# Kernel optimization log

Hardware: AMD Instinct MI355X
Metric: run time of the kernel (lower is better)

Reference implementation:

```python
import jax, jax.numpy as jnp
import numpy as np
from jax import lax

DIM = 96
D_STATE = 16
D_CONV = 4
EXPAND = 2
D_INNER = EXPAND * DIM           # 192
DT_RANK = (DIM + 15) // 16       # 6
EPS = 1e-5


def _upsample2x_align_corners(x):
    # bilinear, align_corners=True, scale_factor=2 (matches nn.Upsample)
    B, C, H, W = x.shape
    def lin_idx(n_in, n_out):
        pos = jnp.arange(n_out) * ((n_in - 1) / (n_out - 1))
        i0 = jnp.floor(pos).astype(jnp.int32)
        i1 = jnp.minimum(i0 + 1, n_in - 1)
        w = (pos - i0).astype(x.dtype)
        return i0, i1, w
    r0, r1, rw = lin_idx(H, 2 * H)
    c0, c1, cw = lin_idx(W, 2 * W)
    xr = x[:, :, r0, :] * (1 - rw)[None, None, :, None] + x[:, :, r1, :] * rw[None, None, :, None]
    return xr[:, :, :, c0] * (1 - cw) + xr[:, :, :, c1] * cw


def _conv2d(x, w, b, pad):
    y = lax.conv_general_dilated(x, w, (1, 1), [(pad, pad), (pad, pad)],
                                 dimension_numbers=('NCHW', 'OIHW', 'NCHW'))
    return y + b[None, :, None, None]


def _instance_norm(x):
    m = x.mean(axis=(2, 3), keepdims=True)
    v = x.var(axis=(2, 3), keepdims=True)
    return (x - m) * lax.rsqrt(v + EPS)


def _selective_scan(u, dt, A, Bm, Cm, D):
    # u, dt: [B,L,Din]; Bm, Cm: [B,L,N]; A: [Din,N]; D: [Din]
    def step(h, inp):
        u_t, dt_t, B_t, C_t = inp                       # [B,Din],[B,Din],[B,N],[B,N]
        dA = jnp.exp(dt_t[..., None] * A)               # [B,Din,N]
        h = h * dA + (dt_t * u_t)[..., None] * B_t[:, None, :]
        y = jnp.einsum('bdn,bn->bd', h, C_t)
        return h, y
    Bsz, L, Din = u.shape
    h0 = jnp.zeros((Bsz, Din, A.shape[1]), u.dtype)
    xs = (u.swapaxes(0, 1), dt.swapaxes(0, 1), Bm.swapaxes(0, 1), Cm.swapaxes(0, 1))
    _, ys = lax.scan(step, h0, xs)                      # ys: [L,B,Din]
    return ys.swapaxes(0, 1) + u * D


def _mamba(xseq, in_proj_w, conv1d_w, conv1d_b, x_proj_w, dt_proj_w, dt_proj_b,
           A_log, D, out_proj_w):
    # xseq: [B,L,dim]
    xz = xseq @ in_proj_w.T                             # [B,L,2*Din]
    xin, z = jnp.split(xz, 2, axis=-1)
    xc = xin.swapaxes(1, 2)                             # [B,Din,L]
    xc = lax.conv_general_dilated(xc, conv1d_w, (1,), [(D_CONV - 1, 0)],
                                  dimension_numbers=('NCH', 'OIH', 'NCH'),
                                  feature_group_count=D_INNER)
    xc = xc + conv1d_b[None, :, None]
    u = jax.nn.silu(xc.swapaxes(1, 2))                  # [B,L,Din]
    x_dbl = u @ x_proj_w.T                              # [B,L,dt_rank+2N]
    dt, Bm, Cm = jnp.split(x_dbl, [DT_RANK, DT_RANK + D_STATE], axis=-1)
    dt = jax.nn.softplus(dt @ dt_proj_w.T + dt_proj_b)  # [B,L,Din]
    A = -jnp.exp(A_log)                                 # [Din,N]
    y = _selective_scan(u, dt, A, Bm, Cm, D)
    y = y * jax.nn.silu(z)
    return y @ out_proj_w.T                             # [B,L,dim]


def setup_inputs() -> dict:
    key = jax.random.key(0)
    ks = jax.random.split(key, 16)
    s = 0.05
    inp = {
        'x': jax.random.normal(ks[0], (2, DIM, 64, 64), jnp.float32),
        'Hx': jax.random.normal(ks[1], (2, DIM * 2, 128, 128), jnp.float32),
        'conv1_w': jax.random.normal(ks[2], (DIM, DIM * 3, 1, 1), jnp.float32) * s,
        'conv1_b': jax.random.normal(ks[3], (DIM,), jnp.float32) * s,
        'conv2_w': jax.random.normal(ks[4], (DIM, DIM, 3, 3), jnp.float32) * s,
        'conv2_b': jax.random.normal(ks[5], (DIM,), jnp.float32) * s,
        'conv3_w': jax.random.normal(ks[6], (DIM, DIM, 1, 1), jnp.float32) * s,
        'conv3_b': jax.random.normal(ks[7], (DIM,), jnp.float32) * s,
        'in_proj_w': jax.random.normal(ks[8], (2 * D_INNER, DIM), jnp.float32) * s,
        'conv1d_w': jax.random.normal(ks[9], (D_INNER, 1, D_CONV), jnp.float32) * s,
        'conv1d_b': jax.random.normal(ks[10], (D_INNER,), jnp.float32) * s,
        'x_proj_w': jax.random.normal(ks[11], (DT_RANK + 2 * D_STATE, D_INNER), jnp.float32) * s,
        'dt_proj_w': jax.random.normal(ks[12], (D_INNER, DT_RANK), jnp.float32) * s,
        'dt_proj_b': jax.random.normal(ks[13], (D_INNER,), jnp.float32) * 0.1,
        'A_log': jnp.log(jnp.tile(jnp.arange(1, D_STATE + 1, dtype=jnp.float32)[None, :], (D_INNER, 1))),
        'D': jnp.ones((D_INNER,), jnp.float32),
        'out_proj_w': jax.random.normal(ks[14], (DIM, D_INNER), jnp.float32) * s,
    }
    return inp


def reference(x, Hx, conv1_w, conv1_b, conv2_w, conv2_b, conv3_w, conv3_b,
              in_proj_w, conv1d_w, conv1d_b, x_proj_w, dt_proj_w, dt_proj_b,
              A_log, D, out_proj_w):
    up = _upsample2x_align_corners(x)                   # [B,dim,H,W]
    cat = jnp.concatenate([up, Hx], axis=1)             # [B,3*dim,H,W]
    h = _conv2d(cat, conv1_w, conv1_b, 0)
    h = _conv2d(h, conv2_w, conv2_b, 1)
    h = _conv2d(h, conv3_w, conv3_b, 0)
    Lx = jax.nn.selu(_instance_norm(h))                 # [B,dim,H,W]
    B, C, H, W = Lx.shape
    seq = Lx.reshape(B, C, H * W).swapaxes(1, 2)        # [B,L,dim]
    y = _mamba(seq, in_proj_w, conv1d_w, conv1d_b, x_proj_w, dt_proj_w,
               dt_proj_b, A_log, D, out_proj_w)
    return y.swapaxes(1, 2).reshape(B, C, H, W) + Lx
```

## Files before the change

### kernel.cpp

```cpp
#include <hip/hip_runtime.h>
#include <hip/hip_bf16.h>
#include <math.h>

#define LSEQ 16384
#define DIN  192
#define GCH  512
#define TCH  32

typedef float f4v __attribute__((ext_vector_type(4)));
typedef short s8v __attribute__((ext_vector_type(8)));
typedef unsigned short u16x8 __attribute__((ext_vector_type(8)));

__device__ __forceinline__ float siluf(float x) { return __fdividef(x, 1.0f + __expf(-x)); }
__device__ __forceinline__ float fexp2(float x) {
#if __has_builtin(__builtin_amdgcn_exp2f)
  return __builtin_amdgcn_exp2f(x);
#else
  return __expf(x * 0.69314718056f);
#endif
}
__device__ __forceinline__ unsigned short f2bf(float f) {
  unsigned int u = __float_as_uint(f);
  unsigned int r = (u + 0x7FFFu + ((u >> 16) & 1u)) >> 16;
  return (unsigned short)r;
}
__device__ __forceinline__ float bf2f(unsigned short s) {
  return __uint_as_float(((unsigned int)s) << 16);
}

__global__ __launch_bounds__(256) void k_packw(const float* __restrict__ c1w,
    const float* __restrict__ c2w, const float* __restrict__ c3w,
    const float* __restrict__ Win, const float* __restrict__ Wx,
    const float* __restrict__ Wout, unsigned short* __restrict__ P) {
  int i = blockIdx.x * 256 + threadIdx.x;
  if (i >= 184320) return;
  if (i < 27648) { P[i] = f2bf(c1w[i]); return; }
  int j = i - 27648;
  if (j < 82944) {
    int cc = j / 27648, r = j - cc * 27648;
    int kk = r / 3072, r2 = r - kk * 3072;
    int oc = r2 >> 5, icl = r2 & 31;
    int ky = kk / 3, kx = kk - ky * 3;
    P[i] = f2bf(c2w[((oc * 96 + cc * 32 + icl) * 3 + ky) * 3 + kx]);
    return;
  }
  j -= 82944;
  if (j < 9216) { P[i] = f2bf(c3w[j]); return; }
  j -= 9216;
  if (j < 36864) { P[i] = f2bf(Win[j]); return; }
  j -= 36864;
  if (j < 9216) {
    int oc = j / 192, k = j - oc * 192;
    P[i] = (oc < 38) ? f2bf(Wx[oc * 192 + k]) : (unsigned short)0;
    return;
  }
  j -= 9216;
  P[i] = f2bf(Wout[j]);
}

#define SRC_PLANAR2 0
#define SRC_ROWS    1
#define SRC_UPCAT   2
#define OUT_BF16R    0
#define OUT_F32P     1
#define OUT_F32R     2
#define OUT_F32P_RES 4
#define OUT_XZ       5

template<int SM, int OM, int NT>
__global__ __launch_bounds__(256) void k_gemm(
    const void* __restrict__ xa, const void* __restrict__ xb, int CA,
    const unsigned short* __restrict__ Wp, const float* __restrict__ bias,
    void* __restrict__ outv, void* __restrict__ outv2, const float* __restrict__ resid,
    int K, int ostride, int ng) {
  __shared__ unsigned short x_t[128 * 96];
  __shared__ unsigned short w_t[NT * 16 * 96];
  Wp += (size_t)blockIdx.y * 96 * K;
  int pxg0 = blockIdx.x * 128;
  int b = pxg0 >> 14, px_in0 = pxg0 & 16383;
  int tid = threadIdx.x, lane = tid & 63, wv = tid >> 6;
  int r = lane & 15, q = lane >> 4;
  f4v acc[2][NT];
#pragma unroll
  for (int mi = 0; mi < 2; mi++)
#pragma unroll
    for (int n = 0; n < NT; n++) acc[mi][n] = (f4v)0.0f;
  int nchunk = K / 96;
  for (int kc = 0; kc < nchunk; kc++) {
    for (int t = tid; t < NT * 16 * 12; t += 256) {
      int row = t / 12, u8 = t - row * 12;
      *(u16x8*)&w_t[row * 96 + u8 * 8] = *(const u16x8*)&Wp[(size_t)row * K + kc * 96 + u8 * 8];
    }
    if (SM == SRC_PLANAR2) {
      const float* A0 = (const float*)xa;
      const float* A1 = (const float*)xb;
      int CB = K - CA;
      for (int t = tid; t < 3072; t += 256) {
        int px4 = t / 96, c_l = t - px4 * 96;
        int c = kc * 96 + c_l;
        const float* sp = (c < CA) ? (A0 + ((size_t)b * CA + c) * LSEQ + px_in0 + px4 * 4)
                                   : (A1 + ((size_t)b * CB + (c - CA)) * LSEQ + px_in0 + px4 * 4);
        float4 v = *(const float4*)sp;
        x_t[(px4 * 4 + 0) * 96 + c_l] = f2bf(v.x);
        x_t[(px4 * 4 + 1) * 96 + c_l] = f2bf(v.y);
        x_t[(px4 * 4 + 2) * 96 + c_l] = f2bf(v.z);
        x_t[(px4 * 4 + 3) * 96 + c_l] = f2bf(v.w);
      }
    } else if (SM == SRC_UPCAT) {
      const float* X0 = (const float*)xa;
      const float* HX = (const float*)xb;
      for (int t = tid; t < 3072; t += 256) {
        int px4 = t / 96, c_l = t - px4 * 96;
        int c = kc * 96 + c_l;
        int pxl = px4 * 4;
        if (c < 96) {
          int pxg = px_in0 + pxl;
          int oh = pxg >> 7, ow0 = pxg & 127;
          float pr = oh * (63.0f / 127.0f);
          int r0 = (int)pr; float rw = pr - (float)r0; int r1 = min(r0 + 1, 63);
          const float* rp0 = X0 + ((size_t)b * 96 + c) * 4096 + r0 * 64;
          const float* rp1 = X0 + ((size_t)b * 96 + c) * 4096 + r1 * 64;
#pragma unroll
          for (int g = 0; g < 4; g++) {
            int ow = ow0 + g;
            float pc = ow * (63.0f / 127.0f);
            int c0 = (int)pc; float cw = pc - (float)c0; int c1 = min(c0 + 1, 63);
            float v00 = rp0[c0], v01 = rp0[c1], v10 = rp1[c0], v11 = rp1[c1];
            float top = v00 + (v10 - v00) * rw;
            float bot = v01 + (v11 - v01) * rw;
            x_t[(pxl + g) * 96 + c_l] = f2bf(top + (bot - top) * cw);
          }
        } else {
          float4 v = *(const float4*)&HX[((size_t)b * 192 + (c - 96)) * LSEQ + px_in0 + pxl];
          x_t[(pxl + 0) * 96 + c_l] = f2bf(v.x);
          x_t[(pxl + 1) * 96 + c_l] = f2bf(v.y);
          x_t[(pxl + 2) * 96 + c_l] = f2bf(v.z);
          x_t[(pxl + 3) * 96 + c_l] = f2bf(v.w);
        }
      }
    } else {
      const unsigned short* X = (const unsigned short*)xa;
      for (int t = tid; t < 1536; t += 256) {
        int rr = t / 12, u8 = t - rr * 12;
        *(u16x8*)&x_t[rr * 96 + u8 * 8] =
            *(const u16x8*)&X[(size_t)(pxg0 + rr) * K + kc * 96 + u8 * 8];
      }
    }
    __syncthreads();
#pragma unroll
    for (int k0 = 0; k0 < 96; k0 += 32) {
      s8v a0 = *(const s8v*)&x_t[((wv * 2 + 0) * 16 + r) * 96 + k0 + q * 8];
      s8v a1 = *(const s8v*)&x_t[((wv * 2 + 1) * 16 + r) * 96 + k0 + q * 8];
#pragma unroll
      for (int n = 0; n < NT; n++) {
        s8v bb = *(const s8v*)&w_t[(n * 16 + r) * 96 + k0 + q * 8];
        acc[0][n] = __builtin_amdgcn_mfma_f32_16x16x32_bf16(a0, bb, acc[0][n], 0, 0, 0);
        acc[1][n] = __builtin_amdgcn_mfma_f32_16x16x32_bf16(a1, bb, acc[1][n], 0, 0, 0);
      }
    }
    __syncthreads();
  }
#pragma unroll
  for (int mi = 0; mi < 2; mi++) {
    int pxl = (wv * 2 + mi) * 16 + q * 4;
    int pxg = pxg0 + pxl;
#pragma unroll
    for (int n = 0; n < NT; n++) {
      int oc = n * 16 + r;
      if (OM == OUT_BF16R) {
        float bv = bias[oc];
        unsigned short* O = (unsigned short*)outv;
#pragma unroll
        for (int g = 0; g < 4; g++)
          O[(size_t)(pxg + g) * 96 + oc] = f2bf(acc[mi][n][g] + bv);
      } else if (OM == OUT_F32P) {
        float bv = bias[oc];
        float* O = (float*)outv;
        float4 o = make_float4(acc[mi][n][0] + bv, acc[mi][n][1] + bv,
                               acc[mi][n][2] + bv, acc[mi][n][3] + bv);
        *(float4*)&O[((size_t)b * 96 + oc) * LSEQ + px_in0 + pxl] = o;
      } else if (OM == OUT_F32P_RES) {
        float* O = (float*)outv;
        size_t ad = ((size_t)b * 96 + oc) * LSEQ + px_in0 + pxl;
        float4 rv = *(const float4*)&resid[ad];
        float4 o = make_float4(acc[mi][n][0] + rv.x, acc[mi][n][1] + rv.y,
                               acc[mi][n][2] + rv.z, acc[mi][n][3] + rv.w);
        *(float4*)&O[ad] = o;
      } else if (OM == OUT_F32R) {
        float* O = (float*)outv;
        int ocg = blockIdx.y * 96 + oc;
        if (ocg < ng) {
#pragma unroll
          for (int g = 0; g < 4; g++)
            O[(size_t)(pxg + g) * ostride + ocg] = acc[mi][n][g];
        }
      } else {
        int ocg = (blockIdx.y & 1) * 96 + oc;
        if (blockIdx.y < 2) {
          float* O = (float*)outv;
#pragma unroll
          for (int g = 0; g < 4; g++)
            O[(size_t)(pxg + g) * 192 + ocg] = acc[mi][n][g];
        } else {
          unsigned short* O = (unsigned short*)outv2;
#pragma unroll
          for (int g = 0; g < 4; g++)
            O[(size_t)(pxg + g) * 192 + ocg] = f2bf(acc[mi][n][g]);
        }
      }
    }
  }
}

__global__ __launch_bounds__(256) void k_conv3x3m(const unsigned short* __restrict__ X,
    const unsigned short* __restrict__ Wp2, const float* __restrict__ bias,
    unsigned short* __restrict__ out) {
  __shared__ unsigned short in_t[3 * 68 * 32];
  __shared__ unsigned short w_t[9 * 96 * 32];
  int bi = blockIdx.x;
  int hx = bi & 1, y = (bi >> 1) & 127, b = bi >> 8;
  int px0 = hx * 64;
  int tid = threadIdx.x, lane = tid & 63, wv = tid >> 6;
  int r = lane & 15, q = lane >> 4;
  f4v acc[6];
#pragma unroll
  for (int n = 0; n < 6; n++) acc[n] = (f4v)0.0f;
  for (int cc = 0; cc < 3; cc++) {
    for (int t = tid; t < 3456; t += 256)
      *(u16x8*)&w_t[t * 8] = *(const u16x8*)&Wp2[cc * 27648 + t * 8];
    for (int t = tid; t < 792; t += 256) {
      int row = t / 264, rem = t - row * 264;
      int c_l = rem >> 2, icq = rem & 3;
      int gy = y - 1 + row, gx = px0 - 1 + c_l;
      u16x8 v = {0, 0, 0, 0, 0, 0, 0, 0};
      if (gy >= 0 && gy < 128 && gx >= 0 && gx < 128)
        v = *(const u16x8*)&X[(((size_t)b * 128 + gy) * 128 + gx) * 96 + cc * 32 + icq * 8];
      *(u16x8*)&in_t[(row * 68 + c_l) * 32 + icq * 8] = v;
    }
    __syncthreads();
#pragma unroll
    for (int kk = 0; kk < 9; kk++) {
      int ky = kk / 3, kx = kk - ky * 3;
      s8v a = *(const s8v*)&in_t[(ky * 68 + wv * 16 + r + kx) * 32 + q * 8];
#pragma unroll
      for (int n = 0; n < 6; n++) {
        s8v bb = *(const s8v*)&w_t[(kk * 96 + n * 16 + r) * 32 + q * 8];
        acc[n] = __builtin_amdgcn_mfma_f32_16x16x32_bf16(a, bb, acc[n], 0, 0, 0);
      }
    }
    __syncthreads();
  }
  size_t rowbase = ((size_t)b * 128 + y) * 128 + px0 + wv * 16 + q * 4;
#pragma unroll
  for (int n = 0; n < 6; n++) {
    int oc = n * 16 + r;
    float bv = bias[oc];
#pragma unroll
    for (int g = 0; g < 4; g++)
      out[(rowbase + g) * 96 + oc] = f2bf(acc[n][g] + bv);
  }
}

__global__ __launch_bounds__(256) void k_stats(const float* __restrict__ h, float* __restrict__ stats) {
  int bc = blockIdx.x;
  const float* p = h + (size_t)bc * LSEQ;
  float s = 0.f, ss = 0.f;
  for (int i = threadIdx.x; i < LSEQ; i += 256) { float v = p[i]; s += v; ss = fmaf(v, v, ss); }
  __shared__ float rs[256], rss[256];
  int tid = threadIdx.x;
  rs[tid] = s; rss[tid] = ss; __syncthreads();
  for (int o = 128; o > 0; o >>= 1) {
    if (tid < o) { rs[tid] += rs[tid + o]; rss[tid] += rss[tid + o]; }
    __syncthreads();
  }
  if (tid == 0) {
    float m = rs[0] * (1.0f / LSEQ);
    float var = rss[0] * (1.0f / LSEQ) - m * m;
    stats[bc * 2] = m;
    stats[bc * 2 + 1] = rsqrtf(fmaxf(var, 0.f) + 1e-5f);
  }
}

__device__ __forceinline__ float seluf(float v) {
  const float kS = 1.0507009873554805f, kSA = 1.0507009873554805f * 1.6732632423543772f;
  return v > 0.f ? kS * v : kSA * (__expf(v) - 1.f);
}
__global__ __launch_bounds__(256) void k_normselu2(const float* __restrict__ h,
    const float* __restrict__ stats, float* __restrict__ Lx, unsigned short* __restrict__ LxR) {
  __shared__ float tile[96 * 65];
  int px0 = blockIdx.x * 64, b = blockIdx.y;
  int tid = threadIdx.x;
  for (int t = tid; t < 1536; t += 256) {
    int c = t >> 4, p4 = t & 15;
    size_t ga = ((size_t)b * 96 + c) * LSEQ + px0 + p4 * 4;
    float4 v = *(const float4*)&h[ga];
    float m = stats[(b * 96 + c) * 2], rv = stats[(b * 96 + c) * 2 + 1];
    v.x = seluf((v.x - m) * rv);
    v.y = seluf((v.y - m) * rv);
    v.z = seluf((v.z - m) * rv);
    v.w = seluf((v.w - m) * rv);
    *(float4*)&Lx[ga] = v;
    tile[c * 65 + p4 * 4 + 0] = v.x;
    tile[c * 65 + p4 * 4 + 1] = v.y;
    tile[c * 65 + p4 * 4 + 2] = v.z;
    tile[c * 65 + p4 * 4 + 3] = v.w;
  }
  __syncthreads();
  for (int t = tid; t < 768; t += 256) {
    int px = t / 12, c8 = t - px * 12;
    u16x8 o;
#pragma unroll
    for (int jj = 0; jj < 8; jj++) o[jj] = f2bf(tile[(c8 * 8 + jj) * 65 + px]);
    *(u16x8*)&LxR[((size_t)b * LSEQ + px0 + px) * 96 + c8 * 8] = o;
  }
}

__global__ __launch_bounds__(256) void k_conv1d(const float* __restrict__ xzx,
    const float* __restrict__ w1d, const float* __restrict__ b1d,
    float* __restrict__ u, unsigned short* __restrict__ uR) {
  int gid = blockIdx.x * 256 + threadIdx.x;
  if (gid >= 2 * LSEQ * DIN) return;
  int d = gid % DIN, bl = gid / DIN;
  int l = bl & (LSEQ - 1);
  float4 w = *(const float4*)&w1d[d * 4];
  float wv[4] = {w.x, w.y, w.z, w.w};
  float acc = b1d[d];
#pragma unroll
  for (int k = 0; k < 4; k++) {
    int lk = l - 3 + k;
    if (lk >= 0) acc = fmaf(wv[k], xzx[(size_t)(bl - 3 + k) * DIN + d], acc);
  }
  float s = siluf(acc);
  u[gid] = s;
  uR[gid] = f2bf(s);
}

__global__ __launch_bounds__(192, 3) void k_scanA(const float* __restrict__ u,
    const float* __restrict__ xdbl, const float* __restrict__ Wdt,
    const float* __restrict__ bdt, const float* __restrict__ Alog,
    float* __restrict__ chA, float* __restrict__ chB) {
  int b = blockIdx.y, g = blockIdx.x, d = threadIdx.x;
  __shared__ float Bs[TCH * 16], Dts[TCH * 8];
  for (int i = d; i < TCH * 16; i += 192) {
    int t = i >> 4, n = i & 15;
    Bs[i] = xdbl[(size_t)(b * LSEQ + g * TCH + t) * 38 + 6 + n];
  }
  for (int i = d; i < TCH * 6; i += 192) {
    int t = i / 6, c = i - t * 6;
    Dts[t * 8 + c] = xdbl[(size_t)(b * LSEQ + g * TCH + t) * 38 + c];
  }
  float ac2[16];
#pragma unroll
  for (int n = 0; n < 16; n++) ac2[n] = -__expf(Alog[d * 16 + n]) * 1.44269504f;
  float wdt[6];
#pragma unroll
  for (int c = 0; c < 6; c++) wdt[c] = Wdt[d * 6 + c];
  float bd = bdt[d];
  size_t base0 = (size_t)(b * LSEQ + g * TCH);
  float uu[TCH];
#pragma unroll
  for (int t = 0; t < TCH; t++) uu[t] = u[(base0 + t) * DIN + d];
  __syncthreads();
  float dtv[TCH];
#pragma unroll
  for (int t = 0; t < TCH; t++) {
    float dr = bd;
#pragma unroll
    for (int c = 0; c < 6; c++) dr = fmaf(Dts[t * 8 + c], wdt[c], dr);
    dtv[t] = dr > 20.f ? dr : __logf(1.f + __expf(dr));
  }
  float ap[16], hb[16];
#pragma unroll
  for (int n = 0; n < 16; n++) { ap[n] = 1.f; hb[n] = 0.f; }
#pragma unroll
  for (int t = 0; t < TCH; t++) {
    float du = dtv[t] * uu[t];
    float bs[16];
    const float4* src = (const float4*)&Bs[t * 16];
#pragma unroll
    for (int qq = 0; qq < 4; qq++) {
      float4 v = src[qq];
      bs[qq * 4] = v.x; bs[qq * 4 + 1] = v.y; bs[qq * 4 + 2] = v.z; bs[qq * 4 + 3] = v.w;
    }
#pragma unroll
    for (int n = 0; n < 16; n++) {
      float e = fexp2(dtv[t] * ac2[n]);
      ap[n] *= e;
      hb[n] = fmaf(hb[n], e, du * bs[n]);
    }
  }
  size_t co = ((size_t)(b * GCH + g) * DIN + d) * 16;
#pragma unroll
  for (int qq = 0; qq < 4; qq++) {
    ((float4*)(chA + co))[qq] = make_float4(ap[qq * 4], ap[qq * 4 + 1], ap[qq * 4 + 2], ap[qq * 4 + 3]);
    ((float4*)(chB + co))[qq] = make_float4(hb[qq * 4], hb[qq * 4 + 1], hb[qq * 4 + 2], hb[qq * 4 + 3]);
  }
}

__global__ __launch_bounds__(256) void k_scanB(const float* __restrict__ chA,
    const float* __restrict__ chB, float* __restrict__ h0) {
  __shared__ float sa[16 * 17], sb[16 * 17];
  int blk = blockIdx.x;
  int b = blk / DIN, d = blk - b * DIN;
  int tid = threadIdx.x;
  int seg = tid >> 4, n = tid & 15;
  float ca[32], cb[32];
  float aagg = 1.f, bagg = 0.f;
#pragma unroll 8
  for (int j = 0; j < 32; j++) {
    int g = seg * 32 + j;
    size_t off = ((size_t)(b * GCH + g) * DIN + d) * 16 + n;
    float a = chA[off], bb = chB[off];
    ca[j] = a; cb[j] = bb;
    bagg = fmaf(a, bagg, bb);
    aagg *= a;
  }
  sa[n * 17 + seg] = aagg;
  sb[n * 17 + seg] = bagg;
  __syncthreads();
  if (tid < 16) {
    float pa = 1.f, pb = 0.f;
#pragma unroll
    for (int s = 0; s < 16; s++) {
      float ta = sa[tid * 17 + s], tb = sb[tid * 17 + s];
      sa[tid * 17 + s] = pa;
      sb[tid * 17 + s] = pb;
      pb = fmaf(ta, pb, tb);
      pa *= ta;
    }
  }
  __syncthreads();
  float h = sb[n * 17 + seg];
#pragma unroll 8
  for (int j = 0; j < 32; j++) {
    int g = seg * 32 + j;
    size_t off = ((size_t)(b * GCH + g) * DIN + d) * 16 + n;
    h0[off] = h;
    h = fmaf(ca[j], h, cb[j]);
  }
}

__global__ __launch_bounds__(192, 3) void k_scanC(const float* __restrict__ u,
    const float* __restrict__ xdbl, const float* __restrict__ Wdt,
    const float* __restrict__ bdt, const unsigned short* __restrict__ zR,
    const float* __restrict__ Alog, const float* __restrict__ Dp,
    const float* __restrict__ h0, unsigned short* __restrict__ yR) {
  int b = blockIdx.y, g = blockIdx.x, d = threadIdx.x;
  __shared__ float Bs[TCH * 16], Cs[TCH * 16], Dts[TCH * 8];
  for (int i = d; i < TCH * 16; i += 192) {
    int t = i >> 4, n = i & 15;
    size_t rb = (size_t)(b * LSEQ + g * TCH + t) * 38;
    Bs[i] = xdbl[rb + 6 + n];
    Cs[i] = xdbl[rb + 22 + n];
  }
  for (int i = d; i < TCH * 6; i += 192) {
    int t = i / 6, c = i - t * 6;
    Dts[t * 8 + c] = xdbl[(size_t)(b * LSEQ + g * TCH + t) * 38 + c];
  }
  float ac2[16];
#pragma unroll
  for (int n = 0; n < 16; n++) ac2[n] = -__expf(Alog[d * 16 + n]) * 1.44269504f;
  float wdt[6];
#pragma unroll
  for (int c = 0; c < 6; c++) wdt[c] = Wdt[d * 6 + c];
  float bd = bdt[d];
  float Dd = Dp[d];
  size_t base0 = (size_t)(b * LSEQ + g * TCH);
  float uu[TCH];
#pragma unroll
  for (int t = 0; t < TCH; t++) uu[t] = u[(base0 + t) * DIN + d];
  size_t co = ((size_t)(b * GCH + g) * DIN + d) * 16;
  float h[16];
#pragma unroll
  for (int qq = 0; qq < 4; qq++) {
    float4 v = ((const float4*)(h0 + co))[qq];
    h[qq * 4] = v.x; h[qq * 4 + 1] = v.y; h[qq * 4 + 2] = v.z; h[qq * 4 + 3] = v.w;
  }
  __syncthreads();
  float dtv[TCH];
#pragma unroll
  for (int t = 0; t < TCH; t++) {
    float dr = bd;
#pragma unroll
    for (int c = 0; c < 6; c++) dr = fmaf(Dts[t * 8 + c], wdt[c], dr);
    dtv[t] = dr > 20.f ? dr : __logf(1.f + __expf(dr));
  }
#pragma unroll
  for (int t = 0; t < TCH; t++) {
    float du = dtv[t] * uu[t];
    float zv = bf2f(zR[(base0 + t) * DIN + d]);
    float bs[16], cs[16];
    const float4* sbp = (const float4*)&Bs[t * 16];
    const float4* scp = (const float4*)&Cs[t * 16];
#pragma unroll
    for (int qq = 0; qq < 4; qq++) {
      float4 vb = sbp[qq], vc = scp[qq];
      bs[qq * 4] = vb.x; bs[qq * 4 + 1] = vb.y; bs[qq * 4 + 2] = vb.z; bs[qq * 4 + 3] = vb.w;
      cs[qq * 4] = vc.x; cs[qq * 4 + 1] = vc.y; cs[qq * 4 + 2] = vc.z; cs[qq * 4 + 3] = vc.w;
    }
    float y0 = 0.f, y1 = 0.f, y2 = 0.f, y3 = 0.f;
#pragma unroll
    for (int n = 0; n < 16; n++) {
      float e = fexp2(dtv[t] * ac2[n]);
      h[n] = fmaf(h[n], e, du * bs[n]);
      float p = h[n] * cs[n];
      if ((n & 3) == 0) y0 += p; else if ((n & 3) == 1) y1 += p;
      else if ((n & 3) == 2) y2 += p; else y3 += p;
    }
    float yv = ((y0 + y1) + (y2 + y3)) + uu[t] * Dd;
    yR[(base0 + t) * DIN + d] = f2bf(yv * siluf(zv));
  }
}

extern "C" void kernel_launch(void* const* d_in, const int* in_sizes, int n_in,
                              void* d_out, int out_size, void* d_ws, size_t ws_size,
                              hipStream_t stream) {
  (void)in_sizes; (void)n_in; (void)out_size; (void)ws_size;
  const float* x    = (const float*)d_in[0];
  const float* Hx   = (const float*)d_in[1];
  const float* c1w  = (const float*)d_in[2];
  const float* c1b  = (const float*)d_in[3];
  const float* c2w  = (const float*)d_in[4];
  const float* c2b  = (const float*)d_in[5];
  const float* c3w  = (const float*)d_in[6];
  const float* c3b  = (const float*)d_in[7];
  const float* Win  = (const float*)d_in[8];
  const float* w1d  = (const float*)d_in[9];
  const float* b1d  = (const float*)d_in[10];
  const float* Wx   = (const float*)d_in[11];
  const float* Wdt  = (const float*)d_in[12];
  const float* bdt  = (const float*)d_in[13];
  const float* Alog = (const float*)d_in[14];
  const float* Dp   = (const float*)d_in[15];
  const float* Wout = (const float*)d_in[16];
  float* out = (float*)d_out;

  float* ws = (float*)d_ws;
  const size_t F = (size_t)2 * 96 * LSEQ;
  const size_t Fh = F / 2;

  float*          b_h3 = ws;
  float*          chA  = ws;
  float*          b_Lx = ws + F;
  unsigned short* R1   = (unsigned short*)(ws + 2 * F);
  unsigned short* R2   = (unsigned short*)(ws + 2 * F + Fh);
  float*          xdbl = ws + 2 * F + Fh;
  float*          xzx  = ws + 3 * F;
  float*          chB  = ws + 3 * F;
  float*          h0b  = ws + 4 * F;
  unsigned short* zRb  = (unsigned short*)(ws + 5 * F);
  unsigned short* R3   = (unsigned short*)(ws + 6 * F);
  float*          b_u  = ws + 7 * F;
  unsigned short* Wp   = (unsigned short*)(ws + 9 * F);
  float*          b_st = ws + 9 * F + 92160;

  k_packw<<<dim3(720), dim3(256), 0, stream>>>(c1w, c2w, c3w, Win, Wx, Wout, Wp);
  k_gemm<SRC_UPCAT, OUT_BF16R, 6><<<dim3(256, 1), dim3(256), 0, stream>>>(
      x, Hx, 96, Wp, c1b, R1, nullptr, nullptr, 288, 0, 0);
  k_conv3x3m<<<dim3(512), dim3(256), 0, stream>>>(R1, Wp + 27648, c2b, R2);
  k_gemm<SRC_ROWS, OUT_F32P, 6><<<dim3(256, 1), dim3(256), 0, stream>>>(
      R2, nullptr, 0, Wp + 110592, c3b, b_h3, nullptr, nullptr, 96, 0, 0);
  k_stats<<<dim3(192), dim3(256), 0, stream>>>(b_h3, b_st);
  k_normselu2<<<dim3(256, 2), dim3(256), 0, stream>>>(b_h3, b_st, b_Lx, R1);
  k_gemm<SRC_ROWS, OUT_XZ, 6><<<dim3(256, 4), dim3(256), 0, stream>>>(
      R1, nullptr, 0, Wp + 119808, nullptr, xzx, zRb, nullptr, 96, 192, 0);
  k_conv1d<<<dim3((2 * LSEQ * DIN + 255) / 256), dim3(256), 0, stream>>>(xzx, w1d, b1d, b_u, R3);
  k_gemm<SRC_ROWS, OUT_F32R, 3><<<dim3(256, 1), dim3(256), 0, stream>>>(
      R3, nullptr, 0, Wp + 156672, nullptr, xdbl, nullptr, nullptr, 192, 38, 38);
  k_scanA<<<dim3(GCH, 2), dim3(192), 0, stream>>>(b_u, xdbl, Wdt, bdt, Alog, chA, chB);
  k_scanB<<<dim3(2 * DIN), dim3(256), 0, stream>>>(chA, chB, h0b);
  k_scanC<<<dim3(GCH, 2), dim3(192), 0, stream>>>(b_u, xdbl, Wdt, bdt, zRb, Alog, Dp, h0b, R3);
  k_gemm<SRC_ROWS, OUT_F32P_RES, 6><<<dim3(256, 1), dim3(256), 0, stream>>>(
      R3, nullptr, 0, Wp + 165888, nullptr, out, nullptr, b_Lx, 192, 0, 0);
}
```

Baseline: 347.4 us.

## Precompute upsample-concat into bf16 rows and drop fp32 scan input buffer

The bilinear upsample and concat with Hx now run in a separate kernel that writes a bf16 row-major [px,288] buffer, so the first 1x1 GEMM can use the plain vectorized row loader in place of per-element gather and convert inside its K loop. The conv1d kernel no longer writes an fp32 copy of u, and both scan kernels read the bf16 copy and widen it. This removes one fp32 write and two fp32 reads of the large u tensor and simplifies the GEMM template. In exchange it adds a launch plus a write and read of the concatenated activation, and scan inputs lose precision to bf16.

```diff
diff --git a/kernel.cpp b/kernel.cpp
--- a/kernel.cpp
+++ b/kernel.cpp
@@ -58,18 +58,62 @@
   P[i] = f2bf(Wout[j]);
 }
 
-#define SRC_PLANAR2 0
-#define SRC_ROWS    1
-#define SRC_UPCAT   2
+__global__ __launch_bounds__(256) void k_upcat(const float* __restrict__ x,
+    const float* __restrict__ Hx, unsigned short* __restrict__ UH) {
+  __shared__ float tile[96 * 65];
+  int px0 = blockIdx.x * 64, b = blockIdx.y;
+  int tid = threadIdx.x;
+  for (int cg = 0; cg < 3; cg++) {
+    if (cg == 0) {
+      int oh = px0 >> 7, owbase = px0 & 127;
+      float pr = oh * (63.0f / 127.0f);
+      int r0 = (int)pr; float rw = pr - (float)r0; int r1 = min(r0 + 1, 63);
+      for (int t = tid; t < 1536; t += 256) {
+        int c = t >> 4, p4 = t & 15;
+        const float* rp0 = x + ((size_t)b * 96 + c) * 4096 + r0 * 64;
+        const float* rp1 = x + ((size_t)b * 96 + c) * 4096 + r1 * 64;
+#pragma unroll
+        for (int g = 0; g < 4; g++) {
+          int ow = owbase + p4 * 4 + g;
+          float pc = ow * (63.0f / 127.0f);
+          int c0 = (int)pc; float cw = pc - (float)c0; int c1 = min(c0 + 1, 63);
+          float v00 = rp0[c0], v01 = rp0[c1], v10 = rp1[c0], v11 = rp1[c1];
+          float top = v00 + (v10 - v00) * rw;
+          float bot = v01 + (v11 - v01) * rw;
+          tile[c * 65 + p4 * 4 + g] = top + (bot - top) * cw;
+        }
+      }
+    } else {
+      for (int t = tid; t < 1536; t += 256) {
+        int c = t >> 4, p4 = t & 15;
+        float4 v = *(const float4*)&Hx[((size_t)b * 192 + (cg - 1) * 96 + c) * LSEQ + px0 + p4 * 4];
+        tile[c * 65 + p4 * 4 + 0] = v.x;
+        tile[c * 65 + p4 * 4 + 1] = v.y;
+        tile[c * 65 + p4 * 4 + 2] = v.z;
+        tile[c * 65 + p4 * 4 + 3] = v.w;
+      }
+    }
+    __syncthreads();
+    for (int t = tid; t < 768; t += 256) {
+      int px = t / 12, c8 = t - px * 12;
+      u16x8 o;
+#pragma unroll
+      for (int jj = 0; jj < 8; jj++) o[jj] = f2bf(tile[(c8 * 8 + jj) * 65 + px]);
+      *(u16x8*)&UH[((size_t)b * LSEQ + px0 + px) * 288 + cg * 96 + c8 * 8] = o;
+    }
+    __syncthreads();
+  }
+}
+
 #define OUT_BF16R    0
 #define OUT_F32P     1
 #define OUT_F32R     2
 #define OUT_F32P_RES 4
 #define OUT_XZ       5
 
-template<int SM, int OM, int NT>
+template<int OM, int NT>
 __global__ __launch_bounds__(256) void k_gemm(
-    const void* __restrict__ xa, const void* __restrict__ xb, int CA,
+    const unsigned short* __restrict__ X,
     const unsigned short* __restrict__ Wp, const float* __restrict__ bias,
     void* __restrict__ outv, void* __restrict__ outv2, const float* __restrict__ resid,
     int K, int ostride, int ng) {
@@ -91,60 +135,10 @@
       int row = t / 12, u8 = t - row * 12;
       *(u16x8*)&w_t[row * 96 + u8 * 8] = *(const u16x8*)&Wp[(size_t)row * K + kc * 96 + u8 * 8];
     }
-    if (SM == SRC_PLANAR2) {
-      const float* A0 = (const float*)xa;
-      const float* A1 = (const float*)xb;
-      int CB = K - CA;
-      for (int t = tid; t < 3072; t += 256) {
-        int px4 = t / 96, c_l = t - px4 * 96;
-        int c = kc * 96 + c_l;
-        const float* sp = (c < CA) ? (A0 + ((size_t)b * CA + c) * LSEQ + px_in0 + px4 * 4)
-                                   : (A1 + ((size_t)b * CB + (c - CA)) * LSEQ + px_in0 + px4 * 4);
-        float4 v = *(const float4*)sp;
-        x_t[(px4 * 4 + 0) * 96 + c_l] = f2bf(v.x);
-        x_t[(px4 * 4 + 1) * 96 + c_l] = f2bf(v.y);
-        x_t[(px4 * 4 + 2) * 96 + c_l] = f2bf(v.z);
-        x_t[(px4 * 4 + 3) * 96 + c_l] = f2bf(v.w);
-      }
-    } else if (SM == SRC_UPCAT) {
-      const float* X0 = (const float*)xa;
-      const float* HX = (const float*)xb;
-      for (int t = tid; t < 3072; t += 256) {
-        int px4 = t / 96, c_l = t - px4 * 96;
-        int c = kc * 96 + c_l;
-        int pxl = px4 * 4;
-        if (c < 96) {
-          int pxg = px_in0 + pxl;
-          int oh = pxg >> 7, ow0 = pxg & 127;
-          float pr = oh * (63.0f / 127.0f);
-          int r0 = (int)pr; float rw = pr - (float)r0; int r1 = min(r0 + 1, 63);
-          const float* rp0 = X0 + ((size_t)b * 96 + c) * 4096 + r0 * 64;
-          const float* rp1 = X0 + ((size_t)b * 96 + c) * 4096 + r1 * 64;
-#pragma unroll
-          for (int g = 0; g < 4; g++) {
-            int ow = ow0 + g;
-            float pc = ow * (63.0f / 127.0f);
-            int c0 = (int)pc; float cw = pc - (float)c0; int c1 = min(c0 + 1, 63);
-            float v00 = rp0[c0], v01 = rp0[c1], v10 = rp1[c0], v11 = rp1[c1];
-            float top = v00 + (v10 - v00) * rw;
-            float bot = v01 + (v11 - v01) * rw;
-            x_t[(pxl + g) * 96 + c_l] = f2bf(top + (bot - top) * cw);
-          }
-        } else {
-          float4 v = *(const float4*)&HX[((size_t)b * 192 + (c - 96)) * LSEQ + px_in0 + pxl];
-          x_t[(pxl + 0) * 96 + c_l] = f2bf(v.x);
-          x_t[(pxl + 1) * 96 + c_l] = f2bf(v.y);
-          x_t[(pxl + 2) * 96 + c_l] = f2bf(v.z);
-          x_t[(pxl + 3) * 96 + c_l] = f2bf(v.w);
-        }
-      }
-    } else {
-      const unsigned short* X = (const unsigned short*)xa;
-      for (int t = tid; t < 1536; t += 256) {
-        int rr = t / 12, u8 = t - rr * 12;
-        *(u16x8*)&x_t[rr * 96 + u8 * 8] =
-            *(const u16x8*)&X[(size_t)(pxg0 + rr) * K + kc * 96 + u8 * 8];
-      }
+    for (int t = tid; t < 1536; t += 256) {
+      int rr = t / 12, u8 = t - rr * 12;
+      *(u16x8*)&x_t[rr * 96 + u8 * 8] =
+          *(const u16x8*)&X[(size_t)(pxg0 + rr) * K + kc * 96 + u8 * 8];
     }
     __syncthreads();
 #pragma unroll
@@ -317,7 +311,7 @@
 
 __global__ __launch_bounds__(256) void k_conv1d(const float* __restrict__ xzx,
     const float* __restrict__ w1d, const float* __restrict__ b1d,
-    float* __restrict__ u, unsigned short* __restrict__ uR) {
+    unsigned short* __restrict__ uR) {
   int gid = blockIdx.x * 256 + threadIdx.x;
   if (gid >= 2 * LSEQ * DIN) return;
   int d = gid % DIN, bl = gid / DIN;
@@ -330,12 +324,10 @@
     int lk = l - 3 + k;
     if (lk >= 0) acc = fmaf(wv[k], xzx[(size_t)(bl - 3 + k) * DIN + d], acc);
   }
-  float s = siluf(acc);
-  u[gid] = s;
-  uR[gid] = f2bf(s);
-}
-
-__global__ __launch_bounds__(192, 3) void k_scanA(const float* __restrict__ u,
+  uR[gid] = f2bf(siluf(acc));
+}
+
+__global__ __launch_bounds__(192, 3) void k_scanA(const unsigned short* __restrict__ uR,
     const float* __restrict__ xdbl, const float* __restrict__ Wdt,
     const float* __restrict__ bdt, const float* __restrict__ Alog,
     float* __restrict__ chA, float* __restrict__ chB) {
@@ -359,7 +351,7 @@
   size_t base0 = (size_t)(b * LSEQ + g * TCH);
   float uu[TCH];
 #pragma unroll
-  for (int t = 0; t < TCH; t++) uu[t] = u[(base0 + t) * DIN + d];
+  for (int t = 0; t < TCH; t++) uu[t] = bf2f(uR[(base0 + t) * DIN + d]);
   __syncthreads();
   float dtv[TCH];
 #pragma unroll
@@ -440,7 +432,7 @@
   }
 }
 
-__global__ __launch_bounds__(192, 3) void k_scanC(const float* __restrict__ u,
+__global__ __launch_bounds__(192, 3) void k_scanC(const unsigned short* __restrict__ uR,
     const float* __restrict__ xdbl, const float* __restrict__ Wdt,
     const float* __restrict__ bdt, const unsigned short* __restrict__ zR,
     const float* __restrict__ Alog, const float* __restrict__ Dp,
@@ -468,7 +460,7 @@
   size_t base0 = (size_t)(b * LSEQ + g * TCH);
   float uu[TCH];
 #pragma unroll
-  for (int t = 0; t < TCH; t++) uu[t] = u[(base0 + t) * DIN + d];
+  for (int t = 0; t < TCH; t++) uu[t] = bf2f(uR[(base0 + t) * DIN + d]);
   size_t co = ((size_t)(b * GCH + g) * DIN + d) * 16;
   float h[16];
 #pragma unroll
@@ -545,31 +537,33 @@
   unsigned short* R1   = (unsigned short*)(ws + 2 * F);
   unsigned short* R2   = (unsigned short*)(ws + 2 * F + Fh);
   float*          xdbl = ws + 2 * F + Fh;
+  unsigned short* UH   = (unsigned short*)(ws + 3 * F);
   float*          xzx  = ws + 3 * F;
   float*          chB  = ws + 3 * F;
+  unsigned short* yRb  = (unsigned short*)(ws + 3 * F);
   float*          h0b  = ws + 4 * F;
   unsigned short* zRb  = (unsigned short*)(ws + 5 * F);
   unsigned short* R3   = (unsigned short*)(ws + 6 * F);
-  float*          b_u  = ws + 7 * F;
-  unsigned short* Wp   = (unsigned short*)(ws + 9 * F);
-  float*          b_st = ws + 9 * F + 92160;
+  unsigned short* Wp   = (unsigned short*)(ws + 7 * F);
+  float*          b_st = ws + 7 * F + 92160;
 
   k_packw<<<dim3(720), dim3(256), 0, stream>>>(c1w, c2w, c3w, Win, Wx, Wout, Wp);
-  k_gemm<SRC_UPCAT, OUT_BF16R, 6><<<dim3(256, 1), dim3(256), 0, stream>>>(
-      x, Hx, 96, Wp, c1b, R1, nullptr, nullptr, 288, 0, 0);
+  k_upcat<<<dim3(256, 2), dim3(256), 0, stream>>>(x, Hx, UH);
+  k_gemm<OUT_BF16R, 6><<<dim3(256, 1), dim3(256), 0, stream>>>(
+      UH, Wp, c1b, R1, nullptr, nullptr, 288, 0, 0);
   k_conv3x3m<<<dim3(512), dim3(256), 0, stream>>>(R1, Wp + 27648, c2b, R2);
-  k_gemm<SRC_ROWS, OUT_F32P, 6><<<dim3(256, 1), dim3(256), 0, stream>>>(
-      R2, nullptr, 0, Wp + 110592, c3b, b_h3, nullptr, nullptr, 96, 0, 0);
+  k_gemm<OUT_F32P, 6><<<dim3(256, 1), dim3(256), 0, stream>>>(
+      R2, Wp + 110592, c3b, b_h3, nullptr, nullptr, 96, 0, 0);
   k_stats<<<dim3(192), dim3(256), 0, stream>>>(b_h3, b_st);
   k_normselu2<<<dim3(256, 2), dim3(256), 0, stream>>>(b_h3, b_st, b_Lx, R1);
-  k_gemm<SRC_ROWS, OUT_XZ, 6><<<dim3(256, 4), dim3(256), 0, stream>>>(
-      R1, nullptr, 0, Wp + 119808, nullptr, xzx, zRb, nullptr, 96, 192, 0);
-  k_conv1d<<<dim3((2 * LSEQ * DIN + 255) / 256), dim3(256), 0, stream>>>(xzx, w1d, b1d, b_u, R3);
-  k_gemm<SRC_ROWS, OUT_F32R, 3><<<dim3(256, 1), dim3(256), 0, stream>>>(
-      R3, nullptr, 0, Wp + 156672, nullptr, xdbl, nullptr, nullptr, 192, 38, 38);
-  k_scanA<<<dim3(GCH, 2), dim3(192), 0, stream>>>(b_u, xdbl, Wdt, bdt, Alog, chA, chB);
+  k_gemm<OUT_XZ, 6><<<dim3(256, 4), dim3(256), 0, stream>>>(
+      R1, Wp + 119808, nullptr, xzx, zRb, nullptr, 96, 192, 0);
+  k_conv1d<<<dim3((2 * LSEQ * DIN + 255) / 256), dim3(256), 0, stream>>>(xzx, w1d, b1d, R3);
+  k_gemm<OUT_F32R, 3><<<dim3(256, 1), dim3(256), 0, stream>>>(
+      R3, Wp + 156672, nullptr, xdbl, nullptr, nullptr, 192, 38, 38);
+  k_scanA<<<dim3(GCH, 2), dim3(192), 0, stream>>>(R3, xdbl, Wdt, bdt, Alog, chA, chB);
   k_scanB<<<dim3(2 * DIN), dim3(256), 0, stream>>>(chA, chB, h0b);
-  k_scanC<<<dim3(GCH, 2), dim3(192), 0, stream>>>(b_u, xdbl, Wdt, bdt, zRb, Alog, Dp, h0b, R3);
-  k_gemm<SRC_ROWS, OUT_F32P_RES, 6><<<dim3(256, 1), dim3(256), 0, stream>>>(
-      R3, nullptr, 0, Wp + 165888, nullptr, out, nullptr, b_Lx, 192, 0, 0);
-}
+  k_scanC<<<dim3(GCH, 2), dim3(192), 0, stream>>>(R3, xdbl, Wdt, bdt, zRb, Alog, Dp, h0b, yRb);
+  k_gemm<OUT_F32P_RES, 6><<<dim3(256, 1), dim3(256), 0, stream>>>(
+      yRb, Wp + 165888, nullptr, out, nullptr, b_Lx, 192, 0, 0);
+}
```

After: 333.9 us. 3.9% less time.
